# Kernel optimization log

Measured on AMD Instinct MI355X. Metric: run time of the kernel, lower is better.

Reference implementation:

```python
import jax, jax.numpy as jnp
import numpy as np

N = 50000
E = 800000
D = 128
EPS = 1e-5


def setup_inputs() -> dict:
    key = jax.random.key(0)
    ks = jax.random.split(key, 12)
    x = jax.random.normal(ks[0], (N, D), dtype=jnp.float32)
    pos = jax.random.normal(ks[1], (N, 3), dtype=jnp.float32)
    edge_index = jax.random.randint(ks[2], (2, E), 0, N, dtype=jnp.int32)
    s_e1 = 1.0 / np.sqrt(2 * D + 1)
    s_d = 1.0 / np.sqrt(D)
    s_n1 = 1.0 / np.sqrt(2 * D)
    return {
        "x": x,
        "pos": pos,
        "edge_index": edge_index,
        "W1e": jax.random.uniform(ks[3], (2 * D + 1, D), jnp.float32, -s_e1, s_e1),
        "b1e": jnp.zeros((D,), jnp.float32),
        "W2e": jax.random.uniform(ks[4], (D, D), jnp.float32, -s_d, s_d),
        "b2e": jnp.zeros((D,), jnp.float32),
        "W1n": jax.random.uniform(ks[5], (2 * D, D), jnp.float32, -s_n1, s_n1),
        "b1n": jnp.zeros((D,), jnp.float32),
        "W2n": jax.random.uniform(ks[6], (D, D), jnp.float32, -s_d, s_d),
        "b2n": jnp.zeros((D,), jnp.float32),
        "gamma": jnp.ones((D,), jnp.float32),
        "beta": jnp.zeros((D,), jnp.float32),
    }


def reference(x, pos, edge_index, W1e, b1e, W2e, b2e, W1n, b1n, W2n, b2n, gamma, beta):
    row, col = edge_index[0], edge_index[1]
    # gather + relative position
    rel_pos = pos[row] - pos[col]                       # [E, 3]
    dist2 = jnp.sum(rel_pos * rel_pos, axis=1, keepdims=True)  # [E, 1]
    edge_input = jnp.concatenate([x[row], x[col], dist2], axis=1)  # [E, 2D+1]
    # 2-layer edge MLP with SiLU activations
    h = jax.nn.silu(edge_input @ W1e + b1e)
    edge_feat = jax.nn.silu(h @ W2e + b2e)              # [E, D]
    # scatter-add aggregation onto source nodes (row)
    agg = jax.ops.segment_sum(edge_feat, row, num_segments=x.shape[0])  # [N, D]
    # 2-layer node MLP (SiLU only after first layer)
    node_in = jnp.concatenate([x, agg], axis=1)         # [N, 2D]
    update = jax.nn.silu(node_in @ W1n + b1n) @ W2n + b2n
    # dropout omitted (inference/eval mode)
    # LayerNorm(x + update)
    y = x + update
    mu = jnp.mean(y, axis=-1, keepdims=True)
    var = jnp.var(y, axis=-1, keepdims=True)
    return (y - mu) * jax.lax.rsqrt(var + EPS) * gamma + beta
```

## Files before the change

kernel.cpp:

```cpp
#include <hip/hip_runtime.h>
#include <hip/hip_bf16.h>
#include <math.h>

#define D 128
#define NND 50000
#define NE 800000
#define NB1 196
#define TPITCH 152

typedef __attribute__((ext_vector_type(8))) short shortx8;
typedef __attribute__((ext_vector_type(4))) float floatx4;

__device__ __forceinline__ float silu_f(float v) {
    return v * __builtin_amdgcn_rcpf(1.0f + __expf(-v));
}
__device__ __forceinline__ unsigned short f2bf(float f) {
    union { float f; unsigned int u; } v; v.f = f;
    unsigned int u = v.u;
    u += 0x7fffu + ((u >> 16) & 1u);
    return (unsigned short)(u >> 16);
}
__device__ __forceinline__ void unpk(unsigned int u, float& lo, float& hi) {
    union { unsigned int x; float f; } a, b;
    a.x = u << 16;
    b.x = u & 0xffff0000u;
    lo = a.f; hi = b.f;
}

__global__ void zero_kernel(float4* __restrict__ p, int n4) {
    int i = blockIdx.x * blockDim.x + threadIdx.x;
    float4 z = make_float4(0.f, 0.f, 0.f, 0.f);
    for (; i < n4; i += gridDim.x * blockDim.x) p[i] = z;
}

__global__ void hist_kernel(const int* __restrict__ ei, int* __restrict__ deg) {
    int e = blockIdx.x * 256 + threadIdx.x;
    atomicAdd(&deg[ei[e]], 1);
}

__global__ void scan1_kernel(const int* __restrict__ deg,
                             int* __restrict__ part, int* __restrict__ bsum) {
    __shared__ int s[256];
    const int tid = threadIdx.x;
    const int i = blockIdx.x * 256 + tid;
    int v = (i < NND) ? deg[i] : 0;
    s[tid] = v;
    __syncthreads();
    #pragma unroll
    for (int off = 1; off < 256; off <<= 1) {
        int t = (tid >= off) ? s[tid - off] : 0;
        __syncthreads();
        s[tid] += t;
        __syncthreads();
    }
    part[i] = s[tid] - v;
    if (tid == 255) bsum[blockIdx.x] = s[255];
}

__global__ void scan2_kernel(const int* __restrict__ bsum, int* __restrict__ boff) {
    __shared__ int s[256];
    const int tid = threadIdx.x;
    int v = (tid < NB1) ? bsum[tid] : 0;
    s[tid] = v;
    __syncthreads();
    #pragma unroll
    for (int off = 1; off < 256; off <<= 1) {
        int t = (tid >= off) ? s[tid - off] : 0;
        __syncthreads();
        s[tid] += t;
        __syncthreads();
    }
    if (tid < NB1) boff[tid] = s[tid] - v;
}

__global__ void scan3_kernel(const int* __restrict__ part, const int* __restrict__ boff,
                             int* __restrict__ rowptr, int* __restrict__ cursor) {
    int i = blockIdx.x * 256 + threadIdx.x;
    if (i < NND) {
        int v = part[i] + boff[i >> 8];
        rowptr[i] = v;
        cursor[i] = v;
    } else if (i == NND) {
        rowptr[NND] = NE;
    }
}

__global__ void scatter_kernel(const int* __restrict__ ei, const float* __restrict__ pos,
                               int* __restrict__ cursor,
                               int* __restrict__ ecol, int* __restrict__ erow,
                               float* __restrict__ ed2) {
    int e = blockIdx.x * 256 + threadIdx.x;
    int r = ei[e], c = ei[NE + e];
    float dx = pos[r * 3 + 0] - pos[c * 3 + 0];
    float dy = pos[r * 3 + 1] - pos[c * 3 + 1];
    float dz = pos[r * 3 + 2] - pos[c * 3 + 2];
    int slot = atomicAdd(&cursor[r], 1);
    ecol[slot] = c;
    erow[slot] = r;
    ed2[slot] = dx * dx + dy * dy + dz * dz;
}

__global__ void wswzall_kernel(const float* __restrict__ W1e, const float* __restrict__ W1n,
                               const float* __restrict__ W2e, const float* __restrict__ W2n,
                               unsigned short* __restrict__ w1f, unsigned short* __restrict__ w1nf,
                               unsigned short* __restrict__ w2f, unsigned short* __restrict__ w2nf,
                               unsigned short* __restrict__ wlf) {
    const int b = blockIdx.x;
    const float* W; unsigned short* Wf; int lb;
    if (b < 128)      { W = W1e; Wf = w1f;  lb = b; }
    else if (b < 256) { W = W1n; Wf = w1nf; lb = b - 128; }
    else if (b < 320) { W = W2e; Wf = w2f;  lb = b - 256; }
    else if (b < 384) { W = W2n; Wf = w2nf; lb = b - 320; }
    else {
        if (threadIdx.x < 128) wlf[threadIdx.x] = f2bf(W1e[256 * D + threadIdx.x]);
        return;
    }
    int f = lb * 256 + threadIdx.x;
    int j    = f & 7;
    int mrow = (f >> 3) & 15;
    int n    = (f >> 7) & 7;
    int rest = f >> 10;
    int quad = rest & 3;
    int ks   = rest >> 2;
    int col = n * 16 + mrow;
    int k   = ks * 32 + quad * 8 + j;
    Wf[f] = f2bf(W[k * D + col]);
}

__global__ void x2bf_kernel(const float4* __restrict__ x4, uint2* __restrict__ xbf) {
    int i = blockIdx.x * 256 + threadIdx.x;
    float4 v = x4[i];
    uint2 o;
    o.x = (unsigned int)f2bf(v.x) | ((unsigned int)f2bf(v.y) << 16);
    o.y = (unsigned int)f2bf(v.z) | ((unsigned int)f2bf(v.w) << 16);
    xbf[i] = o;
}

__global__ __launch_bounds__(256) void precompute_kernel(
        const unsigned short* __restrict__ xbf,
        const unsigned short* __restrict__ w1f,
        const float* __restrict__ b1e,
        unsigned short* __restrict__ A,
        unsigned short* __restrict__ Bm) {
    const int t    = threadIdx.x;
    const int wv   = t >> 6;
    const int lane = t & 63;
    const int mrow = lane & 15;
    const int quad = lane >> 4;
    const int tile = blockIdx.x * 4 + wv;
    if (tile >= 3125) return;
    const int n0 = tile * 16;

    const uint4* xrow = (const uint4*)(xbf + ((size_t)(n0 + mrow) << 7));
    const uint4* wp   = (const uint4*)w1f;

    floatx4 accA[8], accB[8];
    #pragma unroll
    for (int n = 0; n < 8; ++n) {
        accA[n] = (floatx4){0.f, 0.f, 0.f, 0.f};
        accB[n] = (floatx4){0.f, 0.f, 0.f, 0.f};
    }

    #pragma unroll
    for (int s = 0; s < 4; ++s) {
        union { uint4 u; shortx8 v; } af;
        af.u = xrow[s * 4 + quad];
        const int baseA = (s * 4 + quad) * 128 + mrow;
        const int baseB = ((s + 4) * 4 + quad) * 128 + mrow;
        #pragma unroll
        for (int n = 0; n < 8; ++n) {
            union { uint4 u; shortx8 v; } bfA, bfB;
            bfA.u = wp[baseA + n * 16];
            bfB.u = wp[baseB + n * 16];
            accA[n] = __builtin_amdgcn_mfma_f32_16x16x32_bf16(af.v, bfA.v, accA[n], 0, 0, 0);
            accB[n] = __builtin_amdgcn_mfma_f32_16x16x32_bf16(af.v, bfB.v, accB[n], 0, 0, 0);
        }
    }

    float bb[8];
    #pragma unroll
    for (int n = 0; n < 8; ++n) bb[n] = b1e[n * 16 + mrow];

    #pragma unroll
    for (int reg = 0; reg < 4; ++reg) {
        const int node = n0 + quad * 4 + reg;
        #pragma unroll
        for (int n = 0; n < 8; ++n) {
            const int col = n * 16 + mrow;
            A[(size_t)node * D + col]  = f2bf(accA[n][reg] + bb[n]);
            Bm[(size_t)node * D + col] = f2bf(accB[n][reg]);
        }
    }
}

__global__ __launch_bounds__(256) void edgemlp_kernel(
        const unsigned short* __restrict__ Abf,
        const unsigned short* __restrict__ Bbf,
        const int* __restrict__ erow,
        const int* __restrict__ ecol,
        const float* __restrict__ ed2,
        const unsigned short* __restrict__ wlf,
        const unsigned short* __restrict__ W2f,
        const float* __restrict__ b2e,
        unsigned short* __restrict__ ef) {
    const int t    = threadIdx.x;
    const int wv   = t >> 6;
    const int lane = t & 63;
    const int mrow = lane & 15;
    const int quad = lane >> 4;
    const int tile = blockIdx.x * 4 + wv;
    const int e0   = tile * 16;
    const int eme  = e0 + mrow;

    const int   r  = erow[eme];
    const int   c  = ecol[eme];
    const float d2 = ed2[eme];

    const uint4* arow = (const uint4*)(Abf + ((size_t)r << 7));
    const uint4* brow = (const uint4*)(Bbf + ((size_t)c << 7));
    const uint4* wlq  = (const uint4*)wlf;
    const uint4* w2p  = (const uint4*)W2f;

    floatx4 acc[8];
    #pragma unroll
    for (int k = 0; k < 8; ++k) acc[k] = (floatx4){0.f, 0.f, 0.f, 0.f};

    #pragma unroll
    for (int s = 0; s < 4; ++s) {
        uint4 au = arow[s * 4 + quad];
        uint4 bu = brow[s * 4 + quad];
        uint4 wu = wlq[s * 4 + quad];

        float a0, a1, a2, a3, a4, a5, a6, a7;
        float q0, q1, q2, q3, q4, q5, q6, q7;
        float w0, w1, w2, w3, w4, w5, w6, w7;
        unpk(au.x, a0, a1); unpk(au.y, a2, a3);
        unpk(au.z, a4, a5); unpk(au.w, a6, a7);
        unpk(bu.x, q0, q1); unpk(bu.y, q2, q3);
        unpk(bu.z, q4, q5); unpk(bu.w, q6, q7);
        unpk(wu.x, w0, w1); unpk(wu.y, w2, w3);
        unpk(wu.z, w4, w5); unpk(wu.w, w6, w7);

        float h0 = silu_f(fmaf(d2, w0, a0 + q0));
        float h1 = silu_f(fmaf(d2, w1, a1 + q1));
        float h2 = silu_f(fmaf(d2, w2, a2 + q2));
        float h3 = silu_f(fmaf(d2, w3, a3 + q3));
        float h4 = silu_f(fmaf(d2, w4, a4 + q4));
        float h5 = silu_f(fmaf(d2, w5, a5 + q5));
        float h6 = silu_f(fmaf(d2, w6, a6 + q6));
        float h7 = silu_f(fmaf(d2, w7, a7 + q7));

        union { shortx8 v; __hip_bfloat162 p[4]; } af;
        af.p[0] = __float22bfloat162_rn(float2{h0, h1});
        af.p[1] = __float22bfloat162_rn(float2{h2, h3});
        af.p[2] = __float22bfloat162_rn(float2{h4, h5});
        af.p[3] = __float22bfloat162_rn(float2{h6, h7});

        const int base = (s * 4 + quad) * 128 + mrow;
        #pragma unroll
        for (int k = 0; k < 8; ++k) {
            union { uint4 u; shortx8 v; } bf;
            bf.u = w2p[base + k * 16];
            acc[k] = __builtin_amdgcn_mfma_f32_16x16x32_bf16(af.v, bf.v, acc[k], 0, 0, 0);
        }
    }

    float bias[8];
    #pragma unroll
    for (int k = 0; k < 8; ++k) bias[k] = b2e[k * 16 + mrow];

    #pragma unroll
    for (int reg = 0; reg < 4; ++reg) {
        const int edge = e0 + quad * 4 + reg;
        union { uint4 u; __hip_bfloat162 p[4]; } ov;
        #pragma unroll
        for (int n = 0; n < 4; ++n) {
            float v0 = silu_f(acc[2 * n + 0][reg] + bias[2 * n + 0]);
            float v1 = silu_f(acc[2 * n + 1][reg] + bias[2 * n + 1]);
            ov.p[n] = __float22bfloat162_rn(float2{v0, v1});
        }
        *(uint4*)(ef + (((size_t)edge) << 7) + mrow * 8) = ov.u;
    }
}

__global__ __launch_bounds__(256) void aggsum_kernel(
        const unsigned short* __restrict__ ef,
        const int* __restrict__ rowptr,
        float* __restrict__ aggf) {
    const int t    = threadIdx.x;
    const int lane = t & 63;
    const int node = blockIdx.x * 4 + (t >> 6);
    const int start = rowptr[node];
    const int end   = rowptr[node + 1];
    const int sub  = lane >> 4;
    const int j    = lane & 15;

    const uint4* ef4 = (const uint4*)ef;

    float s[8];
    #pragma unroll
    for (int i = 0; i < 8; ++i) s[i] = 0.f;

    for (int e = start; e < end; e += 4) {
        const int  er    = e + sub;
        const bool valid = er < end;
        const int  safe  = valid ? er : start;
        uint4 u = ef4[(size_t)safe * 16 + j];
        float f0, f1, f2, f3, f4, f5, f6, f7;
        unpk(u.x, f0, f1); unpk(u.y, f2, f3);
        unpk(u.z, f4, f5); unpk(u.w, f6, f7);
        if (valid) {
            s[0] += f0; s[1] += f1; s[2] += f2; s[3] += f3;
            s[4] += f4; s[5] += f5; s[6] += f6; s[7] += f7;
        }
    }
    #pragma unroll
    for (int i = 0; i < 8; ++i) {
        s[i] += __shfl_xor(s[i], 16);
        s[i] += __shfl_xor(s[i], 32);
    }
    if (sub == 0) {
        float* dst = aggf + ((size_t)node << 7) + j;
        #pragma unroll
        for (int i = 0; i < 8; ++i) dst[i * 16] = s[i];
    }
}

__global__ __launch_bounds__(256, 2) void edgeagg_kernel(
        const unsigned short* __restrict__ Abf,
        const unsigned short* __restrict__ Bbf,
        const int* __restrict__ rowptr,
        const int* __restrict__ ecol,
        const float* __restrict__ ed2,
        const unsigned short* __restrict__ wlf,
        const unsigned short* __restrict__ W2f,
        const float* __restrict__ b2e,
        float* __restrict__ aggf) {
    const int t    = threadIdx.x;
    const int wv   = t >> 6;
    const int lane = t & 63;
    const int mrow = lane & 15;
    const int quad = lane >> 4;
    const int node = blockIdx.x * 4 + wv;

    const int start = rowptr[node];
    const int d     = rowptr[node + 1] - start;

    const uint4* arow = (const uint4*)(Abf + ((size_t)node << 7));
    const uint4* wlq  = (const uint4*)wlf;
    uint4 au[4], wlu[4];
    #pragma unroll
    for (int s = 0; s < 4; ++s) {
        au[s]  = arow[s * 4 + quad];
        wlu[s] = wlq[s * 4 + quad];
    }
    float bias[8];
    #pragma unroll
    for (int k = 0; k < 8; ++k) bias[k] = b2e[k * 16 + mrow];

    float nacc[8];
    #pragma unroll
    for (int k = 0; k < 8; ++k) nacc[k] = 0.f;

    const uint4* w2p = (const uint4*)W2f;

    for (int tb = 0; tb < d; tb += 16) {
        const int  ei16 = tb + mrow;
        const bool ve   = ei16 < d;
        const int  idx  = start + (ve ? ei16 : 0);
        const int  c    = ecol[idx];
        float d2        = ed2[idx];
        d2 = ve ? d2 : 0.f;
        const uint4* brow = (const uint4*)(Bbf + ((size_t)c << 7));

        floatx4 acc[8];
        #pragma unroll
        for (int k = 0; k < 8; ++k) acc[k] = (floatx4){0.f, 0.f, 0.f, 0.f};

        #pragma unroll
        for (int s = 0; s < 4; ++s) {
            uint4 bu = brow[s * 4 + quad];

            float a0, a1, a2, a3, a4, a5, a6, a7;
            float q0, q1, q2, q3, q4, q5, q6, q7;
            float w0, w1, w2, w3, w4, w5, w6, w7;
            unpk(au[s].x, a0, a1); unpk(au[s].y, a2, a3);
            unpk(au[s].z, a4, a5); unpk(au[s].w, a6, a7);
            unpk(bu.x, q0, q1); unpk(bu.y, q2, q3);
            unpk(bu.z, q4, q5); unpk(bu.w, q6, q7);
            unpk(wlu[s].x, w0, w1); unpk(wlu[s].y, w2, w3);
            unpk(wlu[s].z, w4, w5); unpk(wlu[s].w, w6, w7);

            float h0 = silu_f(fmaf(d2, w0, a0 + q0));
            float h1 = silu_f(fmaf(d2, w1, a1 + q1));
            float h2 = silu_f(fmaf(d2, w2, a2 + q2));
            float h3 = silu_f(fmaf(d2, w3, a3 + q3));
            float h4 = silu_f(fmaf(d2, w4, a4 + q4));
            float h5 = silu_f(fmaf(d2, w5, a5 + q5));
            float h6 = silu_f(fmaf(d2, w6, a6 + q6));
            float h7 = silu_f(fmaf(d2, w7, a7 + q7));

            union { shortx8 v; __hip_bfloat162 p[4]; } af;
            af.p[0] = __float22bfloat162_rn(float2{h0, h1});
            af.p[1] = __float22bfloat162_rn(float2{h2, h3});
            af.p[2] = __float22bfloat162_rn(float2{h4, h5});
            af.p[3] = __float22bfloat162_rn(float2{h6, h7});

            const int base = (s * 4 + quad) * 128 + mrow;
            #pragma unroll
            for (int k = 0; k < 8; ++k) {
                union { uint4 u; shortx8 v; } bf;
                bf.u = w2p[base + k * 16];
                acc[k] = __builtin_amdgcn_mfma_f32_16x16x32_bf16(af.v, bf.v, acc[k], 0, 0, 0);
            }
        }

        #pragma unroll
        for (int reg = 0; reg < 4; ++reg) {
            const bool vr = (tb + quad * 4 + reg) < d;
            #pragma unroll
            for (int k = 0; k < 8; ++k)
                nacc[k] += vr ? silu_f(acc[k][reg] + bias[k]) : 0.f;
        }
    }

    #pragma unroll
    for (int k = 0; k < 8; ++k) {
        float v = nacc[k];
        v += __shfl_xor(v, 16);
        v += __shfl_xor(v, 32);
        nacc[k] = v;
    }
    const int n8a = quad * 2, n8b = quad * 2 + 1;
    aggf[(size_t)node * D + n8a * 16 + mrow] = nacc[n8a];
    aggf[(size_t)node * D + n8b * 16 + mrow] = nacc[n8b];
}

__global__ __launch_bounds__(64) void node_kernel(
        const unsigned short* __restrict__ xbf,
        const float* __restrict__ aggf,
        const unsigned short* __restrict__ w1nf,
        const float* __restrict__ b1n,
        const unsigned short* __restrict__ w2nf,
        const float* __restrict__ b2n,
        const float* __restrict__ x,
        const float* __restrict__ gamma,
        const float* __restrict__ beta,
        float* __restrict__ out) {
    __shared__ __align__(16) unsigned short ts[16 * TPITCH];
    const int lane = threadIdx.x;
    const int mrow = lane & 15;
    const int quad = lane >> 4;
    const int n0 = blockIdx.x * 16;

    const uint4*  xrow  = (const uint4*)(xbf + ((size_t)(n0 + mrow) << 7));
    const float4* growf = (const float4*)(aggf + ((size_t)(n0 + mrow) << 7));
    const uint4*  w1p   = (const uint4*)w1nf;
    const uint4*  w2p   = (const uint4*)w2nf;

    floatx4 acc[8];
    #pragma unroll
    for (int n = 0; n < 8; ++n) {
        float b = b1n[n * 16 + mrow];
        acc[n] = (floatx4){b, b, b, b};
    }

    #pragma unroll
    for (int s = 0; s < 4; ++s) {
        union { uint4 u; shortx8 v; } af;
        af.u = xrow[s * 4 + quad];
        const int base = (s * 4 + quad) * 128 + mrow;
        #pragma unroll
        for (int n = 0; n < 8; ++n) {
            union { uint4 u; shortx8 v; } bf;
            bf.u = w1p[base + n * 16];
            acc[n] = __builtin_amdgcn_mfma_f32_16x16x32_bf16(af.v, bf.v, acc[n], 0, 0, 0);
        }
    }
    #pragma unroll
    for (int s = 0; s < 4; ++s) {
        float4 g0 = growf[(s * 4 + quad) * 2 + 0];
        float4 g1 = growf[(s * 4 + quad) * 2 + 1];
        union { shortx8 v; __hip_bfloat162 p[4]; } af;
        af.p[0] = __float22bfloat162_rn(float2{g0.x, g0.y});
        af.p[1] = __float22bfloat162_rn(float2{g0.z, g0.w});
        af.p[2] = __float22bfloat162_rn(float2{g1.x, g1.y});
        af.p[3] = __float22bfloat162_rn(float2{g1.z, g1.w});
        const int base = ((s + 4) * 4 + quad) * 128 + mrow;
        #pragma unroll
        for (int n = 0; n < 8; ++n) {
            union { uint4 u; shortx8 v; } bf;
            bf.u = w1p[base + n * 16];
            acc[n] = __builtin_amdgcn_mfma_f32_16x16x32_bf16(af.v, bf.v, acc[n], 0, 0, 0);
        }
    }

    #pragma unroll
    for (int reg = 0; reg < 4; ++reg) {
        const int m = quad * 4 + reg;
        #pragma unroll
        for (int n = 0; n < 8; ++n)
            ts[m * TPITCH + n * 16 + mrow] = f2bf(silu_f(acc[n][reg]));
    }
    __syncthreads();

    floatx4 acc2[8];
    #pragma unroll
    for (int n = 0; n < 8; ++n) {
        float b = b2n[n * 16 + mrow];
        acc2[n] = (floatx4){b, b, b, b};
    }
    #pragma unroll
    for (int s = 0; s < 4; ++s) {
        shortx8 af2 = *(const shortx8*)((const char*)ts +
                        mrow * (TPITCH * 2) + (s * 4 + quad) * 16);
        const int base = (s * 4 + quad) * 128 + mrow;
        #pragma unroll
        for (int n = 0; n < 8; ++n) {
            union { uint4 u; shortx8 v; } bf;
            bf.u = w2p[base + n * 16];
            acc2[n] = __builtin_amdgcn_mfma_f32_16x16x32_bf16(af2, bf.v, acc2[n], 0, 0, 0);
        }
    }

    float g[8], bt[8];
    #pragma unroll
    for (int n = 0; n < 8; ++n) {
        g[n]  = gamma[n * 16 + mrow];
        bt[n] = beta[n * 16 + mrow];
    }
    #pragma unroll
    for (int reg = 0; reg < 4; ++reg) {
        const int node = n0 + quad * 4 + reg;
        float u[8];
        float s1 = 0.f, s2 = 0.f;
        #pragma unroll
        for (int n = 0; n < 8; ++n) {
            u[n] = acc2[n][reg] + x[(size_t)node * D + n * 16 + mrow];
            s1 += u[n];
            s2 += u[n] * u[n];
        }
        #pragma unroll
        for (int off = 1; off < 16; off <<= 1) {
            s1 += __shfl_xor(s1, off);
            s2 += __shfl_xor(s2, off);
        }
        const float mu  = s1 * (1.f / 128.f);
        const float var = s2 * (1.f / 128.f) - mu * mu;
        const float rs  = rsqrtf(var + 1e-5f);
        #pragma unroll
        for (int n = 0; n < 8; ++n)
            out[(size_t)node * D + n * 16 + mrow] = (u[n] - mu) * rs * g[n] + bt[n];
    }
}

extern "C" void kernel_launch(void* const* d_in, const int* in_sizes, int n_in,
                              void* d_out, int out_size, void* d_ws, size_t ws_size,
                              hipStream_t stream) {
    const float* x     = (const float*)d_in[0];
    const float* pos   = (const float*)d_in[1];
    const int*   ei    = (const int*)d_in[2];
    const float* W1e   = (const float*)d_in[3];
    const float* b1e   = (const float*)d_in[4];
    const float* W2e   = (const float*)d_in[5];
    const float* b2e   = (const float*)d_in[6];
    const float* W1n   = (const float*)d_in[7];
    const float* b1n   = (const float*)d_in[8];
    const float* W2n   = (const float*)d_in[9];
    const float* b2n   = (const float*)d_in[10];
    const float* gamma = (const float*)d_in[11];
    const float* beta  = (const float*)d_in[12];
    float* out = (float*)d_out;

    int*            deg    = (int*)d_ws;
    int*            part   = deg + 50176;
    int*            bsum   = part + 50176;
    int*            boff   = bsum + 256;
    int*            rowptr = boff + 256;
    int*            cursor = rowptr + 50004;
    int*            ecol   = cursor + 50000;
    int*            erow   = ecol + NE;
    float*          ed2    = (float*)(erow + NE);
    unsigned short* Abf    = (unsigned short*)(ed2 + NE);
    unsigned short* Bbf    = Abf + (size_t)NND * D;
    unsigned short* xbf    = Bbf + (size_t)NND * D;
    unsigned short* w1f    = xbf + (size_t)NND * D;
    unsigned short* w1nf   = w1f + 256 * D;
    unsigned short* w2f    = w1nf + 256 * D;
    unsigned short* w2nf   = w2f + D * D;
    unsigned short* wlf    = w2nf + D * D;
    unsigned short* ef     = wlf + 128;

    const size_t need_big = (size_t)((char*)(ef + (size_t)NE * D) - (char*)d_ws);
    const bool bigws = ws_size >= need_big;

    float* aggf = bigws ? (float*)Abf : (float*)ef;

    zero_kernel<<<49, 256, 0, stream>>>((float4*)deg, 50176 / 4);

    hist_kernel<<<NE / 256, 256, 0, stream>>>(ei, deg);
    scan1_kernel<<<NB1, 256, 0, stream>>>(deg, part, bsum);
    scan2_kernel<<<1, 256, 0, stream>>>(bsum, boff);
    scan3_kernel<<<197, 256, 0, stream>>>(part, boff, rowptr, cursor);
    scatter_kernel<<<NE / 256, 256, 0, stream>>>(ei, pos, cursor, ecol, erow, ed2);

    wswzall_kernel<<<385, 256, 0, stream>>>(W1e, W1n, W2e, W2n,
                                            w1f, w1nf, w2f, w2nf, wlf);
    x2bf_kernel<<<(NND * D / 4) / 256, 256, 0, stream>>>((const float4*)x, (uint2*)xbf);

    precompute_kernel<<<782, 256, 0, stream>>>(xbf, w1f, b1e, Abf, Bbf);

    if (bigws) {
        edgemlp_kernel<<<NE / 16 / 4, 256, 0, stream>>>(Abf, Bbf, erow, ecol, ed2,
                                                        wlf, w2f, b2e, ef);
        aggsum_kernel<<<NND / 4, 256, 0, stream>>>(ef, rowptr, aggf);
    } else {
        edgeagg_kernel<<<NND / 4, 256, 0, stream>>>(Abf, Bbf, rowptr, ecol, ed2,
                                                    wlf, w2f, b2e, aggf);
    }

    node_kernel<<<NND / 16, 64, 0, stream>>>(xbf, aggf, w1nf, b1n, w2nf, b2n,
                                             x, gamma, beta, out);
}
```

Before: 415.6 us.

## Pack edge metadata into uint4 and fuse x bf16 conversion into consumers

The scatter kernel now writes col, row and squared distance into one 16-byte packed record per edge instead of three separate arrays, so each edge-consuming kernel does a single vector load. The separate x-to-bf16 conversion kernel is removed; precompute_kernel and node_kernel read fp32 x directly and convert in registers. edgemlp_kernel also gets a launch-bounds occupancy hint. In exchange, x is read twice as fp32 instead of once as bf16, and the packed records carry an unused padding word.

```diff
diff --git a/kernel.cpp b/kernel.cpp
--- a/kernel.cpp
+++ b/kernel.cpp
@@ -87,17 +87,20 @@
 
 __global__ void scatter_kernel(const int* __restrict__ ei, const float* __restrict__ pos,
                                int* __restrict__ cursor,
-                               int* __restrict__ ecol, int* __restrict__ erow,
-                               float* __restrict__ ed2) {
+                               uint4* __restrict__ epack) {
     int e = blockIdx.x * 256 + threadIdx.x;
     int r = ei[e], c = ei[NE + e];
     float dx = pos[r * 3 + 0] - pos[c * 3 + 0];
     float dy = pos[r * 3 + 1] - pos[c * 3 + 1];
     float dz = pos[r * 3 + 2] - pos[c * 3 + 2];
+    float d2 = dx * dx + dy * dy + dz * dz;
     int slot = atomicAdd(&cursor[r], 1);
-    ecol[slot] = c;
-    erow[slot] = r;
-    ed2[slot] = dx * dx + dy * dy + dz * dz;
+    uint4 v;
+    v.x = (unsigned int)c;
+    v.y = (unsigned int)r;
+    v.z = __float_as_uint(d2);
+    v.w = 0u;
+    epack[slot] = v;
 }
 
 __global__ void wswzall_kernel(const float* __restrict__ W1e, const float* __restrict__ W1n,
@@ -127,17 +130,8 @@
     Wf[f] = f2bf(W[k * D + col]);
 }
 
-__global__ void x2bf_kernel(const float4* __restrict__ x4, uint2* __restrict__ xbf) {
-    int i = blockIdx.x * 256 + threadIdx.x;
-    float4 v = x4[i];
-    uint2 o;
-    o.x = (unsigned int)f2bf(v.x) | ((unsigned int)f2bf(v.y) << 16);
-    o.y = (unsigned int)f2bf(v.z) | ((unsigned int)f2bf(v.w) << 16);
-    xbf[i] = o;
-}
-
 __global__ __launch_bounds__(256) void precompute_kernel(
-        const unsigned short* __restrict__ xbf,
+        const float* __restrict__ x,
         const unsigned short* __restrict__ w1f,
         const float* __restrict__ b1e,
         unsigned short* __restrict__ A,
@@ -151,7 +145,7 @@
     if (tile >= 3125) return;
     const int n0 = tile * 16;
 
-    const uint4* xrow = (const uint4*)(xbf + ((size_t)(n0 + mrow) << 7));
+    const float4* xrow = (const float4*)(x + ((size_t)(n0 + mrow) << 7));
     const uint4* wp   = (const uint4*)w1f;
 
     floatx4 accA[8], accB[8];
@@ -163,8 +157,13 @@
 
     #pragma unroll
     for (int s = 0; s < 4; ++s) {
-        union { uint4 u; shortx8 v; } af;
-        af.u = xrow[s * 4 + quad];
+        float4 xa = xrow[(s * 4 + quad) * 2 + 0];
+        float4 xb = xrow[(s * 4 + quad) * 2 + 1];
+        union { shortx8 v; __hip_bfloat162 p[4]; } af;
+        af.p[0] = __float22bfloat162_rn(float2{xa.x, xa.y});
+        af.p[1] = __float22bfloat162_rn(float2{xa.z, xa.w});
+        af.p[2] = __float22bfloat162_rn(float2{xb.x, xb.y});
+        af.p[3] = __float22bfloat162_rn(float2{xb.z, xb.w});
         const int baseA = (s * 4 + quad) * 128 + mrow;
         const int baseB = ((s + 4) * 4 + quad) * 128 + mrow;
         #pragma unroll
@@ -193,12 +192,10 @@
     }
 }
 
-__global__ __launch_bounds__(256) void edgemlp_kernel(
+__global__ __launch_bounds__(256, 2) void edgemlp_kernel(
         const unsigned short* __restrict__ Abf,
         const unsigned short* __restrict__ Bbf,
-        const int* __restrict__ erow,
-        const int* __restrict__ ecol,
-        const float* __restrict__ ed2,
+        const uint4* __restrict__ epack,
         const unsigned short* __restrict__ wlf,
         const unsigned short* __restrict__ W2f,
         const float* __restrict__ b2e,
@@ -212,9 +209,10 @@
     const int e0   = tile * 16;
     const int eme  = e0 + mrow;
 
-    const int   r  = erow[eme];
-    const int   c  = ecol[eme];
-    const float d2 = ed2[eme];
+    const uint4 ep = epack[eme];
+    const int   c  = (int)ep.x;
+    const int   r  = (int)ep.y;
+    const float d2 = __uint_as_float(ep.z);
 
     const uint4* arow = (const uint4*)(Abf + ((size_t)r << 7));
     const uint4* brow = (const uint4*)(Bbf + ((size_t)c << 7));
@@ -330,8 +328,7 @@
         const unsigned short* __restrict__ Abf,
         const unsigned short* __restrict__ Bbf,
         const int* __restrict__ rowptr,
-        const int* __restrict__ ecol,
-        const float* __restrict__ ed2,
+        const uint4* __restrict__ epack,
         const unsigned short* __restrict__ wlf,
         const unsigned short* __restrict__ W2f,
         const float* __restrict__ b2e,
@@ -368,8 +365,9 @@
         const int  ei16 = tb + mrow;
         const bool ve   = ei16 < d;
         const int  idx  = start + (ve ? ei16 : 0);
-        const int  c    = ecol[idx];
-        float d2        = ed2[idx];
+        const uint4 ep  = epack[idx];
+        const int  c    = (int)ep.x;
+        float d2        = __uint_as_float(ep.z);
         d2 = ve ? d2 : 0.f;
         const uint4* brow = (const uint4*)(Bbf + ((size_t)c << 7));
 
@@ -437,7 +435,6 @@
 }
 
 __global__ __launch_bounds__(64) void node_kernel(
-        const unsigned short* __restrict__ xbf,
         const float* __restrict__ aggf,
         const unsigned short* __restrict__ w1nf,
         const float* __restrict__ b1n,
@@ -453,7 +450,7 @@
     const int quad = lane >> 4;
     const int n0 = blockIdx.x * 16;
 
-    const uint4*  xrow  = (const uint4*)(xbf + ((size_t)(n0 + mrow) << 7));
+    const float4* xrow  = (const float4*)(x + ((size_t)(n0 + mrow) << 7));
     const float4* growf = (const float4*)(aggf + ((size_t)(n0 + mrow) << 7));
     const uint4*  w1p   = (const uint4*)w1nf;
     const uint4*  w2p   = (const uint4*)w2nf;
@@ -467,8 +464,13 @@
 
     #pragma unroll
     for (int s = 0; s < 4; ++s) {
-        union { uint4 u; shortx8 v; } af;
-        af.u = xrow[s * 4 + quad];
+        float4 xa = xrow[(s * 4 + quad) * 2 + 0];
+        float4 xb = xrow[(s * 4 + quad) * 2 + 1];
+        union { shortx8 v; __hip_bfloat162 p[4]; } af;
+        af.p[0] = __float22bfloat162_rn(float2{xa.x, xa.y});
+        af.p[1] = __float22bfloat162_rn(float2{xa.z, xa.w});
+        af.p[2] = __float22bfloat162_rn(float2{xb.x, xb.y});
+        af.p[3] = __float22bfloat162_rn(float2{xb.z, xb.w});
         const int base = (s * 4 + quad) * 128 + mrow;
         #pragma unroll
         for (int n = 0; n < 8; ++n) {
@@ -578,13 +580,10 @@
     int*            boff   = bsum + 256;
     int*            rowptr = boff + 256;
     int*            cursor = rowptr + 50004;
-    int*            ecol   = cursor + 50000;
-    int*            erow   = ecol + NE;
-    float*          ed2    = (float*)(erow + NE);
-    unsigned short* Abf    = (unsigned short*)(ed2 + NE);
+    uint4*          epack  = (uint4*)(cursor + 50000);
+    unsigned short* Abf    = (unsigned short*)(epack + NE);
     unsigned short* Bbf    = Abf + (size_t)NND * D;
-    unsigned short* xbf    = Bbf + (size_t)NND * D;
-    unsigned short* w1f    = xbf + (size_t)NND * D;
+    unsigned short* w1f    = Bbf + (size_t)NND * D;
     unsigned short* w1nf   = w1f + 256 * D;
     unsigned short* w2f    = w1nf + 256 * D;
     unsigned short* w2nf   = w2f + D * D;
@@ -602,23 +601,22 @@
     scan1_kernel<<<NB1, 256, 0, stream>>>(deg, part, bsum);
     scan2_kernel<<<1, 256, 0, stream>>>(bsum, boff);
     scan3_kernel<<<197, 256, 0, stream>>>(part, boff, rowptr, cursor);
-    scatter_kernel<<<NE / 256, 256, 0, stream>>>(ei, pos, cursor, ecol, erow, ed2);
+    scatter_kernel<<<NE / 256, 256, 0, stream>>>(ei, pos, cursor, epack);
 
     wswzall_kernel<<<385, 256, 0, stream>>>(W1e, W1n, W2e, W2n,
                                             w1f, w1nf, w2f, w2nf, wlf);
-    x2bf_kernel<<<(NND * D / 4) / 256, 256, 0, stream>>>((const float4*)x, (uint2*)xbf);
-
-    precompute_kernel<<<782, 256, 0, stream>>>(xbf, w1f, b1e, Abf, Bbf);
+
+    precompute_kernel<<<782, 256, 0, stream>>>(x, w1f, b1e, Abf, Bbf);
 
     if (bigws) {
-        edgemlp_kernel<<<NE / 16 / 4, 256, 0, stream>>>(Abf, Bbf, erow, ecol, ed2,
+        edgemlp_kernel<<<NE / 16 / 4, 256, 0, stream>>>(Abf, Bbf, epack,
                                                         wlf, w2f, b2e, ef);
         aggsum_kernel<<<NND / 4, 256, 0, stream>>>(ef, rowptr, aggf);
     } else {
-        edgeagg_kernel<<<NND / 4, 256, 0, stream>>>(Abf, Bbf, rowptr, ecol, ed2,
+        edgeagg_kernel<<<NND / 4, 256, 0, stream>>>(Abf, Bbf, rowptr, epack,
                                                     wlf, w2f, b2e, aggf);
     }
 
-    node_kernel<<<NND / 16, 64, 0, stream>>>(xbf, aggf, w1nf, b1n, w2nf, b2n,
+    node_kernel<<<NND / 16, 64, 0, stream>>>(aggf, w1nf, b1n, w2nf, b2n,
                                              x, gamma, beta, out);
 }
```

Measured after the change: 379.1 us. -8.8%, faster.
